# Kernel tuning notes

Measured on AMD Instinct MI355X. Metric: run time of the kernel, lower is better.

The kernel has to match this reference:

```python
import jax, jax.numpy as jnp
import numpy as np

SPATIAL_DIM = 2
N_IN = 4096
N_OUT = 1024
C_IN = 32
C_OUT = 32
FILTER_SEQ = (64, 64)
BATCH = 16


def _grid(num_points):
    # replicates: meshgrid(indexing='xy') of linspace(0,1,n) per dim, dstack, view(-1, d)
    n = int(num_points ** (1.0 / SPATIAL_DIM))
    nodes = np.linspace(0.0, 1.0, n)
    X, Y = np.meshgrid(nodes, nodes, indexing='xy')
    return np.dstack((X, Y)).reshape(-1, SPATIAL_DIM)  # (n^2, 2)


def _cache():
    # replicates QuadConvLayer.cache(): bump-support sparsity pattern
    out_locs = _grid(N_OUT)               # (N_OUT, 2)
    in_nodes = _grid(N_IN)                # (N_IN, 2)
    locs = out_locs[:, None, :] - in_nodes[None, :, :]   # (N_OUT, N_IN, 2)
    bump_arg = np.linalg.norm(locs, axis=2) ** 4
    decay_param = (N_IN / 16.0) ** 2
    mask = bump_arg <= 1.0 / decay_param
    idx = np.argwhere(mask)               # (E, 2), row-major sorted like torch.nonzero
    eval_locs = locs[mask]                # (E, 2)
    return eval_locs.astype(np.float32), idx.astype(np.int64)


def setup_inputs() -> dict:
    key = jax.random.key(0)
    k_feat, k1, k2, k3 = jax.random.split(key, 4)
    eval_locs, eval_indices = _cache()
    # filter MLP G: Linear(2,64,bias=False) -> Sin -> Linear(64,64) -> Sin -> Linear(64, C_IN*C_OUT)
    d0, d1, d2, d3 = SPATIAL_DIM, FILTER_SEQ[0], FILTER_SEQ[1], C_IN * C_OUT
    W1 = jax.random.normal(k1, (d0, d1), jnp.float32) / np.sqrt(d0)
    W2 = jax.random.normal(k2, (d1, d2), jnp.float32) / np.sqrt(d1)
    W3 = jax.random.normal(k3, (d2, d3), jnp.float32) / np.sqrt(d2)
    features = jax.random.normal(k_feat, (BATCH, C_IN, N_IN), jnp.float32)
    return {
        "features": features,
        "W1": W1,
        "W2": W2,
        "W3": W3,
        "eval_locs": jnp.asarray(eval_locs),
        "eval_indices": jnp.asarray(eval_indices),
    }


def reference(features, W1, W2, W3, eval_locs, eval_indices):
    B = features.shape[0]
    E = eval_locs.shape[0]
    seg = eval_indices[:, 0]   # output point per edge (sorted)
    src = eval_indices[:, 1]   # input point per edge
    # filter MLP with Sin activations: (E, 2) -> (E, C_IN, C_OUT)
    h = jnp.sin(eval_locs @ W1)
    h = jnp.sin(h @ W2)
    filt = (h @ W3).reshape(E, C_IN, C_OUT)
    # gather features at source points: (B, C_IN, E)
    gathered = features[:, :, src]
    # faithful to torch: a raw reshape (NOT a transpose) of (B, C_IN, E) -> (B, E, C_IN)
    g = gathered.reshape(B, E, C_IN)
    vals = jnp.einsum('bni,nij->bnj', g, filt)   # (B, E, C_OUT)
    # faithful raw reshape (B, E, C_OUT) -> (B, C_OUT, E)
    vals = vals.reshape(B, C_OUT, E)
    # scatter-sum over edges into output points (segment_coo sum)
    integral = jnp.zeros((B, C_OUT, N_OUT), features.dtype).at[:, :, seg].add(vals)
    return integral
```

## Files before the change

kernel.cpp:

```cpp
#include <hip/hip_runtime.h>
#include <hip/hip_bf16.h>

typedef __bf16 bf16x4  __attribute__((ext_vector_type(4)));
typedef __bf16 bf16x8  __attribute__((ext_vector_type(8)));
typedef __bf16 bf16x16 __attribute__((ext_vector_type(16)));
typedef float  f32x4   __attribute__((ext_vector_type(4)));

#define N_IN   4096
#define N_OUT  1024
#define BATCH  16
#define ROWS   16

#define H1_STR   72
#define H2_STR   72
#define FT_JSTR  40
#define FTH_NSTR 648
#define G_STR    520
#define V_STR    520
#define GSTR2    1048
#define VSTR2    1288
#define FB_FT_NSTR 1288
#define SEG_STR  34

#define WS_W3T_OFF    0
#define WS_W2T_OFF    131072
#define WS_FEATT_OFF  139264
#define WS_NEED       4333568

__global__ void qc_zero_kernel(float* __restrict__ out, int n4) {
    int i = blockIdx.x * blockDim.x + threadIdx.x;
    if (i < n4) ((float4*)out)[i] = make_float4(0.f, 0.f, 0.f, 0.f);
}

__global__ void qc_prep_kernel(const float* __restrict__ w3, const float* __restrict__ w2,
                               __bf16* __restrict__ w3t, __bf16* __restrict__ w2t) {
    int gid = blockIdx.x * blockDim.x + threadIdx.x;
    if (gid < 65536) {
        int k = gid & 63, col = gid >> 6;
        w3t[gid] = (__bf16)w3[k * 1024 + col];
    } else {
        int j = gid - 65536;
        int k = j & 63, col = j >> 6;
        w2t[j] = (__bf16)w2[k * 64 + col];
    }
}

__global__ void qc_prep2_kernel(const float* __restrict__ w3, const float* __restrict__ w2,
                                const float* __restrict__ feat,
                                float* __restrict__ out,
                                __bf16* __restrict__ w3t, __bf16* __restrict__ w2t,
                                __bf16* __restrict__ featT) {
    int bid = blockIdx.x, tid = threadIdx.x;
    if (bid < 512) {
        int i = bid * 256 + tid;
        ((float4*)out)[i] = make_float4(0.f, 0.f, 0.f, 0.f);
    } else if (bid < 768) {
        int gid = (bid - 512) * 256 + tid;
        int k = gid & 63, col = gid >> 6;
        w3t[gid] = (__bf16)w3[k * 1024 + col];
    } else if (bid < 784) {
        int j = (bid - 768) * 256 + tid;
        int k = j & 63, col = j >> 6;
        w2t[j] = (__bf16)w2[k * 64 + col];
    } else {
        int bid2 = bid - 784;
        int c    = bid2 >> 4;
        int src  = (bid2 & 15) * 256 + tid;
        bf16x16 v;
        #pragma unroll
        for (int b = 0; b < 16; ++b)
            v[b] = (__bf16)feat[(b * 32 + c) * N_IN + src];
        __bf16* p = &featT[((size_t)c * N_IN + src) * 16];
        *(bf16x8*)p       = *(bf16x8*)&v;
        *(bf16x8*)(p + 8) = *((bf16x8*)&v + 1);
    }
}

__global__ __launch_bounds__(512, 2)
void qc_fused32_kernel(const __bf16* __restrict__ featT,
                       const float* __restrict__ w1,
                       const float* __restrict__ locs,
                       const int*   __restrict__ eidx,
                       const __bf16* __restrict__ w2t,
                       const __bf16* __restrict__ w3t,
                       float* __restrict__ out,
                       int E)
{
    __shared__ __align__(16) unsigned char region1[41472];
    __shared__ __align__(16) __bf16 h1b[32 * H1_STR];
    __shared__ __align__(16) __bf16 h2b[32 * H2_STR];
    __shared__ unsigned short seg_s[32 * SEG_STR];

    __bf16* gb   = (__bf16*)region1;
    __bf16* ftv  = (__bf16*)region1;
    __bf16* vals = (__bf16*)region1;

    const int tid  = threadIdx.x;
    const int lane = tid & 63;
    const int wv   = tid >> 6;
    const int n0   = blockIdx.x * 32;
    const int t0   = n0 * 32;
    const int ch0  = t0 / E;
    const int m0   = t0 - ch0 * E;

    const int tlb = wv * 128 + lane;
    bf16x16 gvv[2];
    #pragma unroll
    for (int h = 0; h < 2; ++h) {
        int tl = tlb + h * 64;
        int mm = m0 + tl;
        int cc = ch0 + (mm >= E);
        if (mm >= E) mm -= E;
        int2 p = ((const int2*)eidx)[mm];
        seg_s[(tl >> 5) * SEG_STR + (tl & 31)] = (unsigned short)p.x;
        int ccc = cc < 32 ? cc : 31;
        bf16x16 g = *(const bf16x16*)&featT[((size_t)ccc * N_IN + p.y) * 16];
        if (cc >= 32) {
            #pragma unroll
            for (int z = 0; z < 16; ++z) g[z] = (__bf16)0.f;
        }
        gvv[h] = g;
    }

    {
        const int r  = tid >> 4;
        const int j0 = (tid & 15) * 4;
        float lx = 0.f, ly = 0.f;
        int n = n0 + r;
        if (n < E) { lx = locs[n * 2]; ly = locs[n * 2 + 1]; }
        float4 wa = *(const float4*)&w1[j0];
        float4 wb = *(const float4*)&w1[64 + j0];
        __bf16* hp = &h1b[r * H1_STR + j0];
        hp[0] = (__bf16)__sinf(lx * wa.x + ly * wb.x);
        hp[1] = (__bf16)__sinf(lx * wa.y + ly * wb.y);
        hp[2] = (__bf16)__sinf(lx * wa.z + ly * wb.z);
        hp[3] = (__bf16)__sinf(lx * wa.w + ly * wb.w);
    }
    __syncthreads();

    const int ml = lane & 15;
    const int q  = lane >> 4;

    {
        const int rg = (wv >> 2) * 16;
        const int cw = (wv & 3) * 16;
        bf16x8 a0 = *(const bf16x8*)&h1b[(rg + ml) * H1_STR + q * 8];
        bf16x8 a1 = *(const bf16x8*)&h1b[(rg + ml) * H1_STR + 32 + q * 8];
        const __bf16* wp = &w2t[(cw + ml) * 64 + q * 8];
        bf16x8 b0 = *(const bf16x8*)wp;
        bf16x8 b1 = *(const bf16x8*)(wp + 32);
        f32x4 c = {0.f, 0.f, 0.f, 0.f};
        c = __builtin_amdgcn_mfma_f32_16x16x32_bf16(a0, b0, c, 0, 0, 0);
        c = __builtin_amdgcn_mfma_f32_16x16x32_bf16(a1, b1, c, 0, 0, 0);
        #pragma unroll
        for (int g_ = 0; g_ < 4; ++g_)
            h2b[(rg + q * 4 + g_) * H2_STR + cw + ml] = (__bf16)__sinf(c[g_]);
    }

    #pragma unroll
    for (int b = 0; b < 16; ++b) {
        gb[b * GSTR2 + tlb]      = gvv[0][b];
        gb[b * GSTR2 + tlb + 64] = gvv[1][b];
    }
    bf16x8 ag[4];
    #pragma unroll
    for (int rr = 0; rr < 4; ++rr)
        ag[rr] = *(const bf16x8*)&gb[ml * GSTR2 + (wv * 4 + rr) * 32 + q * 8];
    __syncthreads();

    bf16x8 ha00 = *(const bf16x8*)&h2b[ml * H2_STR + q * 8];
    bf16x8 ha01 = *(const bf16x8*)&h2b[ml * H2_STR + 32 + q * 8];
    bf16x8 ha10 = *(const bf16x8*)&h2b[(16 + ml) * H2_STR + q * 8];
    bf16x8 ha11 = *(const bf16x8*)&h2b[(16 + ml) * H2_STR + 32 + q * 8];

    f32x4 c0[4], c1[4];

    {
        f32x4 accA[4], accB[4];
        #pragma unroll
        for (int tt = 0; tt < 4; ++tt) {
            int i_  = wv * 4 + tt;
            int col = i_ * 32 + ml;
            const __bf16* wp = &w3t[col * 64 + q * 8];
            bf16x8 b0 = *(const bf16x8*)wp;
            bf16x8 b1 = *(const bf16x8*)(wp + 32);
            f32x4 cA = {0.f, 0.f, 0.f, 0.f};
            f32x4 cB = {0.f, 0.f, 0.f, 0.f};
            cA = __builtin_amdgcn_mfma_f32_16x16x32_bf16(ha00, b0, cA, 0, 0, 0);
            cA = __builtin_amdgcn_mfma_f32_16x16x32_bf16(ha01, b1, cA, 0, 0, 0);
            cB = __builtin_amdgcn_mfma_f32_16x16x32_bf16(ha10, b0, cB, 0, 0, 0);
            cB = __builtin_amdgcn_mfma_f32_16x16x32_bf16(ha11, b1, cB, 0, 0, 0);
            accA[tt] = cA; accB[tt] = cB;
        }
        #pragma unroll
        for (int g_ = 0; g_ < 4; ++g_) {
            bf16x4 pa, pb;
            #pragma unroll
            for (int tt = 0; tt < 4; ++tt) {
                pa[tt] = (__bf16)accA[tt][g_];
                pb[tt] = (__bf16)accB[tt][g_];
            }
            *(bf16x4*)&ftv[(q * 4 + g_) * FTH_NSTR + ml * FT_JSTR + wv * 4]        = pa;
            *(bf16x4*)&ftv[(16 + q * 4 + g_) * FTH_NSTR + ml * FT_JSTR + wv * 4]   = pb;
        }
    }
    __syncthreads();

    {
        bf16x8 f[4];
        #pragma unroll
        for (int rr = 0; rr < 4; ++rr)
            f[rr] = *(const bf16x8*)&ftv[(wv * 4 + rr) * FTH_NSTR + ml * FT_JSTR + q * 8];
        #pragma unroll
        for (int rr = 0; rr < 4; ++rr) {
            f32x4 z = {0.f, 0.f, 0.f, 0.f};
            c0[rr] = __builtin_amdgcn_mfma_f32_16x16x32_bf16(ag[rr], f[rr], z, 0, 0, 0);
        }
    }
    __syncthreads();

    {
        f32x4 accA[4], accB[4];
        #pragma unroll
        for (int tt = 0; tt < 4; ++tt) {
            int i_  = wv * 4 + tt;
            int col = i_ * 32 + 16 + ml;
            const __bf16* wp = &w3t[col * 64 + q * 8];
            bf16x8 b0 = *(const bf16x8*)wp;
            bf16x8 b1 = *(const bf16x8*)(wp + 32);
            f32x4 cA = {0.f, 0.f, 0.f, 0.f};
            f32x4 cB = {0.f, 0.f, 0.f, 0.f};
            cA = __builtin_amdgcn_mfma_f32_16x16x32_bf16(ha00, b0, cA, 0, 0, 0);
            cA = __builtin_amdgcn_mfma_f32_16x16x32_bf16(ha01, b1, cA, 0, 0, 0);
            cB = __builtin_amdgcn_mfma_f32_16x16x32_bf16(ha10, b0, cB, 0, 0, 0);
            cB = __builtin_amdgcn_mfma_f32_16x16x32_bf16(ha11, b1, cB, 0, 0, 0);
            accA[tt] = cA; accB[tt] = cB;
        }
        #pragma unroll
        for (int g_ = 0; g_ < 4; ++g_) {
            bf16x4 pa, pb;
            #pragma unroll
            for (int tt = 0; tt < 4; ++tt) {
                pa[tt] = (__bf16)accA[tt][g_];
                pb[tt] = (__bf16)accB[tt][g_];
            }
            *(bf16x4*)&ftv[(q * 4 + g_) * FTH_NSTR + ml * FT_JSTR + wv * 4]        = pa;
            *(bf16x4*)&ftv[(16 + q * 4 + g_) * FTH_NSTR + ml * FT_JSTR + wv * 4]   = pb;
        }
    }
    __syncthreads();

    bf16x8 f1[4];
    #pragma unroll
    for (int rr = 0; rr < 4; ++rr)
        f1[rr] = *(const bf16x8*)&ftv[(wv * 4 + rr) * FTH_NSTR + ml * FT_JSTR + q * 8];
    __syncthreads();
    #pragma unroll
    for (int rr = 0; rr < 4; ++rr) {
        f32x4 z = {0.f, 0.f, 0.f, 0.f};
        c1[rr] = __builtin_amdgcn_mfma_f32_16x16x32_bf16(ag[rr], f1[rr], z, 0, 0, 0);
    }
    #pragma unroll
    for (int rr = 0; rr < 4; ++rr) {
        int r = wv * 4 + rr;
        __bf16* vp = &vals[r * FT_JSTR];
        #pragma unroll
        for (int g_ = 0; g_ < 4; ++g_) {
            int b = q * 4 + g_;
            vp[b * VSTR2 + ml]      = (__bf16)c0[rr][g_];
            vp[b * VSTR2 + 16 + ml] = (__bf16)c1[rr][g_];
        }
    }
    __syncthreads();

    {
        const int b   = tid >> 5;
        const int w   = tid & 31;
        const int tl0 = w * 32;
        const __bf16* vp = &vals[b * VSTR2 + w * FT_JSTR];
        bf16x8 v0 = *(const bf16x8*)(vp);
        bf16x8 v1 = *(const bf16x8*)(vp + 8);
        bf16x8 v2 = *(const bf16x8*)(vp + 16);
        bf16x8 v3 = *(const bf16x8*)(vp + 24);
        float vv[32];
        #pragma unroll
        for (int j = 0; j < 8; ++j) {
            vv[j]      = (float)v0[j];
            vv[8 + j]  = (float)v1[j];
            vv[16 + j] = (float)v2[j];
            vv[24 + j] = (float)v3[j];
        }
        int key_prev = -1;
        float acc = 0.f;
        #pragma unroll
        for (int j = 0; j < 32; ++j) {
            int mm2 = m0 + tl0 + j;
            int cc2 = ch0 + (mm2 >= E);
            if (cc2 < 32) {
                int o   = (int)seg_s[w * SEG_STR + j];
                int key = (cc2 << 10) | o;
                if (key != key_prev) {
                    if (key_prev >= 0) atomicAdd(&out[(b << 15) + key_prev], acc);
                    key_prev = key;
                    acc = vv[j];
                } else {
                    acc += vv[j];
                }
            }
        }
        if (key_prev >= 0) atomicAdd(&out[(b << 15) + key_prev], acc);
    }
}

__global__ __launch_bounds__(256, 2)
void qc_main_kernel(const float* __restrict__ feat,
                    const float* __restrict__ w1,
                    const float* __restrict__ w2,
                    const float* __restrict__ locs,
                    const int*   __restrict__ eidx,
                    const __bf16* __restrict__ w3t,
                    float* __restrict__ out,
                    int E)
{
    __shared__ __align__(16) __bf16 h1b[ROWS * H1_STR];
    __shared__ __align__(16) __bf16 h2b[ROWS * H2_STR];
    __shared__ __align__(16) __bf16 ftv[ROWS * FB_FT_NSTR];
    __shared__ __align__(16) __bf16 gb [BATCH * G_STR];
    __shared__ unsigned short seg_s[512];
    __shared__ unsigned short src_s[512];

    const int tid = threadIdx.x;
    const int n0  = blockIdx.x * ROWS;
    const int t0  = n0 * 32;
    const int ch0 = t0 / E;
    const int m0  = t0 - ch0 * E;

    {
        const int r  = tid >> 4;
        const int j0 = (tid & 15) * 4;
        float lx = 0.f, ly = 0.f;
        int n = n0 + r;
        if (n < E) { lx = locs[n * 2]; ly = locs[n * 2 + 1]; }
        float4 wa = *(const float4*)&w1[j0];
        float4 wb = *(const float4*)&w1[64 + j0];
        __bf16* h = &h1b[r * H1_STR + j0];
        h[0] = (__bf16)__sinf(lx * wa.x + ly * wb.x);
        h[1] = (__bf16)__sinf(lx * wa.y + ly * wb.y);
        h[2] = (__bf16)__sinf(lx * wa.z + ly * wb.z);
        h[3] = (__bf16)__sinf(lx * wa.w + ly * wb.w);
    }
    for (int tl = tid; tl < 512; tl += 256) {
        int mm = m0 + tl; if (mm >= E) mm -= E;
        seg_s[tl] = (unsigned short)eidx[mm * 2];
        src_s[tl] = (unsigned short)eidx[mm * 2 + 1];
    }
    __syncthreads();

    {
        const int r  = tid >> 4;
        const int j0 = (tid & 15) * 4;
        float a0 = 0.f, a1 = 0.f, a2 = 0.f, a3 = 0.f;
        const __bf16* h1r = &h1b[r * H1_STR];
        #pragma unroll 8
        for (int k = 0; k < 64; ++k) {
            float h = (float)h1r[k];
            float4 w = *(const float4*)&w2[k * 64 + j0];
            a0 += h * w.x; a1 += h * w.y; a2 += h * w.z; a3 += h * w.w;
        }
        __bf16* h = &h2b[r * H2_STR + j0];
        h[0] = (__bf16)__sinf(a0);
        h[1] = (__bf16)__sinf(a1);
        h[2] = (__bf16)__sinf(a2);
        h[3] = (__bf16)__sinf(a3);
    }
    #pragma unroll 4
    for (int it = 0; it < 32; ++it) {
        int idx = it * 256 + tid;
        int b   = idx >> 9;
        int tl  = idx & 511;
        int mm  = m0 + tl;
        int cc  = ch0 + (mm >= E);
        if (mm >= E) mm -= E;
        float v = 0.f;
        if (cc < 32) v = feat[(b * 32 + cc) * N_IN + (int)src_s[tl]];
        gb[b * G_STR + tl] = (__bf16)v;
    }
    __syncthreads();

    const int lane = tid & 63;
    const int wv   = tid >> 6;
    const int ml   = lane & 15;
    const int q    = lane >> 4;

    {
        bf16x8 a0 = *(const bf16x8*)&h2b[ml * H2_STR + q * 8];
        bf16x8 a1 = *(const bf16x8*)&h2b[ml * H2_STR + 32 + q * 8];
        #pragma unroll
        for (int t = 0; t < 16; ++t) {
            int col = wv * 256 + t * 16 + ml;
            const __bf16* wp = &w3t[col * 64 + q * 8];
            bf16x8 b0 = *(const bf16x8*)wp;
            bf16x8 b1 = *(const bf16x8*)(wp + 32);
            f32x4 c = {0.f, 0.f, 0.f, 0.f};
            c = __builtin_amdgcn_mfma_f32_16x16x32_bf16(a0, b0, c, 0, 0, 0);
            c = __builtin_amdgcn_mfma_f32_16x16x32_bf16(a1, b1, c, 0, 0, 0);
            int i_ = col >> 5, j_ = col & 31;
            __bf16* fp = &ftv[j_ * FT_JSTR + i_];
            fp[(q * 4 + 0) * FB_FT_NSTR] = (__bf16)c[0];
            fp[(q * 4 + 1) * FB_FT_NSTR] = (__bf16)c[1];
            fp[(q * 4 + 2) * FB_FT_NSTR] = (__bf16)c[2];
            fp[(q * 4 + 3) * FB_FT_NSTR] = (__bf16)c[3];
        }
    }
    __syncthreads();

    {
        bf16x8 ag[4], f0[4], f1[4];
        #pragma unroll
        for (int rr = 0; rr < 4; ++rr) {
            int r = wv * 4 + rr;
            ag[rr] = *(const bf16x8*)&gb[ml * G_STR + r * 32 + q * 8];
            f0[rr] = *(const bf16x8*)&ftv[r * FB_FT_NSTR + ml        * FT_JSTR + q * 8];
            f1[rr] = *(const bf16x8*)&ftv[r * FB_FT_NSTR + (16 + ml) * FT_JSTR + q * 8];
        }
        __syncthreads();
        __bf16* valsb = ftv;
        #pragma unroll
        for (int rr = 0; rr < 4; ++rr) {
            int r = wv * 4 + rr;
            f32x4 c0 = {0.f, 0.f, 0.f, 0.f};
            f32x4 c1 = {0.f, 0.f, 0.f, 0.f};
            c0 = __builtin_amdgcn_mfma_f32_16x16x32_bf16(ag[rr], f0[rr], c0, 0, 0, 0);
            c1 = __builtin_amdgcn_mfma_f32_16x16x32_bf16(ag[rr], f1[rr], c1, 0, 0, 0);
            __bf16* vp = &valsb[r * 32];
            #pragma unroll
            for (int g_ = 0; g_ < 4; ++g_) {
                int b = q * 4 + g_;
                vp[b * V_STR + ml]      = (__bf16)c0[g_];
                vp[b * V_STR + 16 + ml] = (__bf16)c1[g_];
            }
        }
    }
    __syncthreads();

    {
        const __bf16* valsb = ftv;
        const int b = tid >> 4;
        const int r = tid & 15;
        const __bf16* vp = &valsb[b * V_STR + r * 32];
        bf16x8 v0 = *(const bf16x8*)(vp);
        bf16x8 v1 = *(const bf16x8*)(vp + 8);
        bf16x8 v2 = *(const bf16x8*)(vp + 16);
        bf16x8 v3 = *(const bf16x8*)(vp + 24);
        float vv[32];
        #pragma unroll
        for (int j = 0; j < 8; ++j) {
            vv[j]      = (float)v0[j];
            vv[8 + j]  = (float)v1[j];
            vv[16 + j] = (float)v2[j];
            vv[24 + j] = (float)v3[j];
        }
        const int tl0 = r * 32;
        int key_prev = -1;
        float acc = 0.f;
        #pragma unroll
        for (int j = 0; j < 32; ++j) {
            int mm = m0 + tl0 + j;
            int cc = ch0 + (mm >= E);
            if (mm >= E) mm -= E;
            if (cc < 32) {
                int o   = (int)seg_s[tl0 + j];
                int key = ((b * 32 + cc) << 10) | o;
                if (key != key_prev) {
                    if (key_prev >= 0) atomicAdd(&out[key_prev], acc);
                    key_prev = key;
                    acc = vv[j];
                } else {
                    acc += vv[j];
                }
            }
        }
        if (key_prev >= 0) atomicAdd(&out[key_prev], acc);
    }
}

extern "C" void kernel_launch(void* const* d_in, const int* in_sizes, int n_in,
                              void* d_out, int out_size, void* d_ws, size_t ws_size,
                              hipStream_t stream)
{
    (void)n_in;
    const float* feat = (const float*)d_in[0];
    const float* w1   = (const float*)d_in[1];
    const float* w2   = (const float*)d_in[2];
    const float* w3   = (const float*)d_in[3];
    const float* locs = (const float*)d_in[4];
    const int*   eidx = (const int*)d_in[5];
    float* out  = (float*)d_out;

    const int E = in_sizes[4] / 2;
    if (E <= 0) return;

    __bf16* w3t   = (__bf16*)((char*)d_ws + WS_W3T_OFF);
    __bf16* w2t   = (__bf16*)((char*)d_ws + WS_W2T_OFF);
    __bf16* featT = (__bf16*)((char*)d_ws + WS_FEATT_OFF);

    if (ws_size >= (size_t)WS_NEED) {
        int nblocks = (E + 31) / 32;
        qc_prep2_kernel<<<1296, 256, 0, stream>>>(w3, w2, feat, out, w3t, w2t, featT);
        qc_fused32_kernel<<<nblocks, 512, 0, stream>>>(featT, w1, locs, eidx, w2t, w3t, out, E);
    } else {
        int n4 = out_size / 4;
        int nblocks = (E + ROWS - 1) / ROWS;
        qc_zero_kernel<<<(n4 + 255) / 256, 256, 0, stream>>>(out, n4);
        qc_prep_kernel<<<272, 256, 0, stream>>>(w3, w2, w3t, w2t);
        qc_main_kernel<<<nblocks, 256, 0, stream>>>(feat, w1, w2, locs, eidx, w3t, out, E);
    }
}
```

Measured before the change: 134.0 us.

## Process two tiles per block with prefetch of next tile's gathers

Each block of the fused kernel now loops over two 32-edge tiles instead of one. W1 and W2 fragments are hoisted out of the loop, and the gather and location loads for the next tile are issued before the scatter-atomic phase of the current tile so their latency overlaps. The launch bound is raised to 4 blocks per CU, and the per-edge channel/key computation in the scatter loop is simplified to a precomputed crossing point. Risks include higher register pressure from the 4-wave occupancy bound, possible spills, and half as many blocks in the grid.

```diff
diff --git a/kernel.cpp b/kernel.cpp
--- a/kernel.cpp
+++ b/kernel.cpp
@@ -21,6 +21,7 @@
 #define VSTR2    1288
 #define FB_FT_NSTR 1288
 #define SEG_STR  34
+#define TPB      2
 
 #define WS_W3T_OFF    0
 #define WS_W2T_OFF    131072
@@ -76,7 +77,7 @@
     }
 }
 
-__global__ __launch_bounds__(512, 2)
+__global__ __launch_bounds__(512, 4)
 void qc_fused32_kernel(const __bf16* __restrict__ featT,
                        const float* __restrict__ w1,
                        const float* __restrict__ locs,
@@ -84,7 +85,7 @@
                        const __bf16* __restrict__ w2t,
                        const __bf16* __restrict__ w3t,
                        float* __restrict__ out,
-                       int E)
+                       int E, int nt)
 {
     __shared__ __align__(16) unsigned char region1[41472];
     __shared__ __align__(16) __bf16 h1b[32 * H1_STR];
@@ -98,217 +99,240 @@
     const int tid  = threadIdx.x;
     const int lane = tid & 63;
     const int wv   = tid >> 6;
-    const int n0   = blockIdx.x * 32;
-    const int t0   = n0 * 32;
-    const int ch0  = t0 / E;
-    const int m0   = t0 - ch0 * E;
-
-    const int tlb = wv * 128 + lane;
-    bf16x16 gvv[2];
-    #pragma unroll
-    for (int h = 0; h < 2; ++h) {
-        int tl = tlb + h * 64;
-        int mm = m0 + tl;
-        int cc = ch0 + (mm >= E);
-        if (mm >= E) mm -= E;
-        int2 p = ((const int2*)eidx)[mm];
-        seg_s[(tl >> 5) * SEG_STR + (tl & 31)] = (unsigned short)p.x;
-        int ccc = cc < 32 ? cc : 31;
-        bf16x16 g = *(const bf16x16*)&featT[((size_t)ccc * N_IN + p.y) * 16];
-        if (cc >= 32) {
-            #pragma unroll
-            for (int z = 0; z < 16; ++z) g[z] = (__bf16)0.f;
-        }
-        gvv[h] = g;
-    }
-
-    {
-        const int r  = tid >> 4;
-        const int j0 = (tid & 15) * 4;
-        float lx = 0.f, ly = 0.f;
-        int n = n0 + r;
+    const int ml   = lane & 15;
+    const int q    = lane >> 4;
+    const int tlb  = wv * 128 + lane;
+
+    const int rA = tid >> 4;
+    const int jA = (tid & 15) * 4;
+    const float4 wa = *(const float4*)&w1[jA];
+    const float4 wb = *(const float4*)&w1[64 + jA];
+    const int rg = (wv >> 2) * 16;
+    const int cw = (wv & 3) * 16;
+    const bf16x8 bw0 = *(const bf16x8*)&w2t[(cw + ml) * 64 + q * 8];
+    const bf16x8 bw1 = *(const bf16x8*)&w2t[(cw + ml) * 64 + 32 + q * 8];
+
+    int tb = blockIdx.x * TPB;
+
+    bf16x16 gvv[2]; int sg0 = 0, sg1 = 0; float lx = 0.f, ly = 0.f;
+
+    auto prefetch = [&](int tbn) {
+        const int t0p  = tbn << 10;
+        const int ch0p = t0p / E;
+        const int m0p  = t0p - ch0p * E;
+        #pragma unroll
+        for (int h = 0; h < 2; ++h) {
+            int tl = tlb + h * 64;
+            int mm = m0p + tl;
+            int cc = ch0p + (mm >= E);
+            if (mm >= E) mm -= E;
+            int2 p = ((const int2*)eidx)[mm];
+            int ccc = cc < 32 ? cc : 31;
+            bf16x16 g = *(const bf16x16*)&featT[((size_t)ccc * N_IN + p.y) * 16];
+            if (cc >= 32) {
+                #pragma unroll
+                for (int z = 0; z < 16; ++z) g[z] = (__bf16)0.f;
+            }
+            gvv[h] = g;
+            if (h == 0) sg0 = p.x; else sg1 = p.x;
+        }
+        int n = (tbn << 5) + rA;
+        lx = 0.f; ly = 0.f;
         if (n < E) { lx = locs[n * 2]; ly = locs[n * 2 + 1]; }
-        float4 wa = *(const float4*)&w1[j0];
-        float4 wb = *(const float4*)&w1[64 + j0];
-        __bf16* hp = &h1b[r * H1_STR + j0];
-        hp[0] = (__bf16)__sinf(lx * wa.x + ly * wb.x);
-        hp[1] = (__bf16)__sinf(lx * wa.y + ly * wb.y);
-        hp[2] = (__bf16)__sinf(lx * wa.z + ly * wb.z);
-        hp[3] = (__bf16)__sinf(lx * wa.w + ly * wb.w);
-    }
-    __syncthreads();
-
-    const int ml = lane & 15;
-    const int q  = lane >> 4;
-
-    {
-        const int rg = (wv >> 2) * 16;
-        const int cw = (wv & 3) * 16;
-        bf16x8 a0 = *(const bf16x8*)&h1b[(rg + ml) * H1_STR + q * 8];
-        bf16x8 a1 = *(const bf16x8*)&h1b[(rg + ml) * H1_STR + 32 + q * 8];
-        const __bf16* wp = &w2t[(cw + ml) * 64 + q * 8];
-        bf16x8 b0 = *(const bf16x8*)wp;
-        bf16x8 b1 = *(const bf16x8*)(wp + 32);
-        f32x4 c = {0.f, 0.f, 0.f, 0.f};
-        c = __builtin_amdgcn_mfma_f32_16x16x32_bf16(a0, b0, c, 0, 0, 0);
-        c = __builtin_amdgcn_mfma_f32_16x16x32_bf16(a1, b1, c, 0, 0, 0);
-        #pragma unroll
-        for (int g_ = 0; g_ < 4; ++g_)
-            h2b[(rg + q * 4 + g_) * H2_STR + cw + ml] = (__bf16)__sinf(c[g_]);
-    }
-
-    #pragma unroll
-    for (int b = 0; b < 16; ++b) {
-        gb[b * GSTR2 + tlb]      = gvv[0][b];
-        gb[b * GSTR2 + tlb + 64] = gvv[1][b];
-    }
-    bf16x8 ag[4];
-    #pragma unroll
-    for (int rr = 0; rr < 4; ++rr)
-        ag[rr] = *(const bf16x8*)&gb[ml * GSTR2 + (wv * 4 + rr) * 32 + q * 8];
-    __syncthreads();
-
-    bf16x8 ha00 = *(const bf16x8*)&h2b[ml * H2_STR + q * 8];
-    bf16x8 ha01 = *(const bf16x8*)&h2b[ml * H2_STR + 32 + q * 8];
-    bf16x8 ha10 = *(const bf16x8*)&h2b[(16 + ml) * H2_STR + q * 8];
-    bf16x8 ha11 = *(const bf16x8*)&h2b[(16 + ml) * H2_STR + 32 + q * 8];
-
-    f32x4 c0[4], c1[4];
-
-    {
-        f32x4 accA[4], accB[4];
-        #pragma unroll
-        for (int tt = 0; tt < 4; ++tt) {
-            int i_  = wv * 4 + tt;
-            int col = i_ * 32 + ml;
-            const __bf16* wp = &w3t[col * 64 + q * 8];
-            bf16x8 b0 = *(const bf16x8*)wp;
-            bf16x8 b1 = *(const bf16x8*)(wp + 32);
-            f32x4 cA = {0.f, 0.f, 0.f, 0.f};
-            f32x4 cB = {0.f, 0.f, 0.f, 0.f};
-            cA = __builtin_amdgcn_mfma_f32_16x16x32_bf16(ha00, b0, cA, 0, 0, 0);
-            cA = __builtin_amdgcn_mfma_f32_16x16x32_bf16(ha01, b1, cA, 0, 0, 0);
-            cB = __builtin_amdgcn_mfma_f32_16x16x32_bf16(ha10, b0, cB, 0, 0, 0);
-            cB = __builtin_amdgcn_mfma_f32_16x16x32_bf16(ha11, b1, cB, 0, 0, 0);
-            accA[tt] = cA; accB[tt] = cB;
-        }
-        #pragma unroll
-        for (int g_ = 0; g_ < 4; ++g_) {
-            bf16x4 pa, pb;
+    };
+
+    prefetch(tb);
+
+    for (int it = 0; it < TPB; ++it, ++tb) {
+        if (tb >= nt) break;
+        const int t0  = tb << 10;
+        const int ch0 = t0 / E;
+        const int m0  = t0 - ch0 * E;
+
+        {
+            __bf16* hp = &h1b[rA * H1_STR + jA];
+            hp[0] = (__bf16)__sinf(lx * wa.x + ly * wb.x);
+            hp[1] = (__bf16)__sinf(lx * wa.y + ly * wb.y);
+            hp[2] = (__bf16)__sinf(lx * wa.z + ly * wb.z);
+            hp[3] = (__bf16)__sinf(lx * wa.w + ly * wb.w);
+        }
+        __syncthreads();
+
+        {
+            bf16x8 a0 = *(const bf16x8*)&h1b[(rg + ml) * H1_STR + q * 8];
+            bf16x8 a1 = *(const bf16x8*)&h1b[(rg + ml) * H1_STR + 32 + q * 8];
+            f32x4 c = {0.f, 0.f, 0.f, 0.f};
+            c = __builtin_amdgcn_mfma_f32_16x16x32_bf16(a0, bw0, c, 0, 0, 0);
+            c = __builtin_amdgcn_mfma_f32_16x16x32_bf16(a1, bw1, c, 0, 0, 0);
+            #pragma unroll
+            for (int g_ = 0; g_ < 4; ++g_)
+                h2b[(rg + q * 4 + g_) * H2_STR + cw + ml] = (__bf16)__sinf(c[g_]);
+        }
+
+        #pragma unroll
+        for (int b = 0; b < 16; ++b) {
+            gb[b * GSTR2 + tlb]      = gvv[0][b];
+            gb[b * GSTR2 + tlb + 64] = gvv[1][b];
+        }
+        seg_s[(tlb >> 5) * SEG_STR + (tlb & 31)] = (unsigned short)sg0;
+        {
+            int tl1 = tlb + 64;
+            seg_s[(tl1 >> 5) * SEG_STR + (tl1 & 31)] = (unsigned short)sg1;
+        }
+        bf16x8 ag[4];
+        #pragma unroll
+        for (int rr = 0; rr < 4; ++rr)
+            ag[rr] = *(const bf16x8*)&gb[ml * GSTR2 + (wv * 4 + rr) * 32 + q * 8];
+        __syncthreads();
+
+        bf16x8 ha00 = *(const bf16x8*)&h2b[ml * H2_STR + q * 8];
+        bf16x8 ha01 = *(const bf16x8*)&h2b[ml * H2_STR + 32 + q * 8];
+        bf16x8 ha10 = *(const bf16x8*)&h2b[(16 + ml) * H2_STR + q * 8];
+        bf16x8 ha11 = *(const bf16x8*)&h2b[(16 + ml) * H2_STR + 32 + q * 8];
+
+        f32x4 c0[4], c1[4];
+
+        {
+            f32x4 accA[4], accB[4];
             #pragma unroll
             for (int tt = 0; tt < 4; ++tt) {
-                pa[tt] = (__bf16)accA[tt][g_];
-                pb[tt] = (__bf16)accB[tt][g_];
-            }
-            *(bf16x4*)&ftv[(q * 4 + g_) * FTH_NSTR + ml * FT_JSTR + wv * 4]        = pa;
-            *(bf16x4*)&ftv[(16 + q * 4 + g_) * FTH_NSTR + ml * FT_JSTR + wv * 4]   = pb;
-        }
-    }
-    __syncthreads();
-
-    {
-        bf16x8 f[4];
+                int i_  = wv * 4 + tt;
+                int col = i_ * 32 + ml;
+                const __bf16* wp = &w3t[col * 64 + q * 8];
+                bf16x8 b0 = *(const bf16x8*)wp;
+                bf16x8 b1 = *(const bf16x8*)(wp + 32);
+                f32x4 cA = {0.f, 0.f, 0.f, 0.f};
+                f32x4 cB = {0.f, 0.f, 0.f, 0.f};
+                cA = __builtin_amdgcn_mfma_f32_16x16x32_bf16(ha00, b0, cA, 0, 0, 0);
+                cA = __builtin_amdgcn_mfma_f32_16x16x32_bf16(ha01, b1, cA, 0, 0, 0);
+                cB = __builtin_amdgcn_mfma_f32_16x16x32_bf16(ha10, b0, cB, 0, 0, 0);
+                cB = __builtin_amdgcn_mfma_f32_16x16x32_bf16(ha11, b1, cB, 0, 0, 0);
+                accA[tt] = cA; accB[tt] = cB;
+            }
+            #pragma unroll
+            for (int g_ = 0; g_ < 4; ++g_) {
+                bf16x4 pa, pb;
+                #pragma unroll
+                for (int tt = 0; tt < 4; ++tt) {
+                    pa[tt] = (__bf16)accA[tt][g_];
+                    pb[tt] = (__bf16)accB[tt][g_];
+                }
+                *(bf16x4*)&ftv[(q * 4 + g_) * FTH_NSTR + ml * FT_JSTR + wv * 4]        = pa;
+                *(bf16x4*)&ftv[(16 + q * 4 + g_) * FTH_NSTR + ml * FT_JSTR + wv * 4]   = pb;
+            }
+        }
+        __syncthreads();
+
+        {
+            bf16x8 f[4];
+            #pragma unroll
+            for (int rr = 0; rr < 4; ++rr)
+                f[rr] = *(const bf16x8*)&ftv[(wv * 4 + rr) * FTH_NSTR + ml * FT_JSTR + q * 8];
+            #pragma unroll
+            for (int rr = 0; rr < 4; ++rr) {
+                f32x4 z = {0.f, 0.f, 0.f, 0.f};
+                c0[rr] = __builtin_amdgcn_mfma_f32_16x16x32_bf16(ag[rr], f[rr], z, 0, 0, 0);
+            }
+        }
+        __syncthreads();
+
+        {
+            f32x4 accA[4], accB[4];
+            #pragma unroll
+            for (int tt = 0; tt < 4; ++tt) {
+                int i_  = wv * 4 + tt;
+                int col = i_ * 32 + 16 + ml;
+                const __bf16* wp = &w3t[col * 64 + q * 8];
+                bf16x8 b0 = *(const bf16x8*)wp;
+                bf16x8 b1 = *(const bf16x8*)(wp + 32);
+                f32x4 cA = {0.f, 0.f, 0.f, 0.f};
+                f32x4 cB = {0.f, 0.f, 0.f, 0.f};
+                cA = __builtin_amdgcn_mfma_f32_16x16x32_bf16(ha00, b0, cA, 0, 0, 0);
+                cA = __builtin_amdgcn_mfma_f32_16x16x32_bf16(ha01, b1, cA, 0, 0, 0);
+                cB = __builtin_amdgcn_mfma_f32_16x16x32_bf16(ha10, b0, cB, 0, 0, 0);
+                cB = __builtin_amdgcn_mfma_f32_16x16x32_bf16(ha11, b1, cB, 0, 0, 0);
+                accA[tt] = cA; accB[tt] = cB;
+            }
+            #pragma unroll
+            for (int g_ = 0; g_ < 4; ++g_) {
+                bf16x4 pa, pb;
+                #pragma unroll
+                for (int tt = 0; tt < 4; ++tt) {
+                    pa[tt] = (__bf16)accA[tt][g_];
+                    pb[tt] = (__bf16)accB[tt][g_];
+                }
+                *(bf16x4*)&ftv[(q * 4 + g_) * FTH_NSTR + ml * FT_JSTR + wv * 4]        = pa;
+                *(bf16x4*)&ftv[(16 + q * 4 + g_) * FTH_NSTR + ml * FT_JSTR + wv * 4]   = pb;
+            }
+        }
+        __syncthreads();
+
+        bf16x8 f1[4];
         #pragma unroll
         for (int rr = 0; rr < 4; ++rr)
-            f[rr] = *(const bf16x8*)&ftv[(wv * 4 + rr) * FTH_NSTR + ml * FT_JSTR + q * 8];
+            f1[rr] = *(const bf16x8*)&ftv[(wv * 4 + rr) * FTH_NSTR + ml * FT_JSTR + q * 8];
+        __syncthreads();
         #pragma unroll
         for (int rr = 0; rr < 4; ++rr) {
             f32x4 z = {0.f, 0.f, 0.f, 0.f};
-            c0[rr] = __builtin_amdgcn_mfma_f32_16x16x32_bf16(ag[rr], f[rr], z, 0, 0, 0);
-        }
-    }
-    __syncthreads();
-
-    {
-        f32x4 accA[4], accB[4];
-        #pragma unroll
-        for (int tt = 0; tt < 4; ++tt) {
-            int i_  = wv * 4 + tt;
-            int col = i_ * 32 + 16 + ml;
-            const __bf16* wp = &w3t[col * 64 + q * 8];
-            bf16x8 b0 = *(const bf16x8*)wp;
-            bf16x8 b1 = *(const bf16x8*)(wp + 32);
-            f32x4 cA = {0.f, 0.f, 0.f, 0.f};
-            f32x4 cB = {0.f, 0.f, 0.f, 0.f};
-            cA = __builtin_amdgcn_mfma_f32_16x16x32_bf16(ha00, b0, cA, 0, 0, 0);
-            cA = __builtin_amdgcn_mfma_f32_16x16x32_bf16(ha01, b1, cA, 0, 0, 0);
-            cB = __builtin_amdgcn_mfma_f32_16x16x32_bf16(ha10, b0, cB, 0, 0, 0);
-            cB = __builtin_amdgcn_mfma_f32_16x16x32_bf16(ha11, b1, cB, 0, 0, 0);
-            accA[tt] = cA; accB[tt] = cB;
-        }
-        #pragma unroll
-        for (int g_ = 0; g_ < 4; ++g_) {
-            bf16x4 pa, pb;
-            #pragma unroll
-            for (int tt = 0; tt < 4; ++tt) {
-                pa[tt] = (__bf16)accA[tt][g_];
-                pb[tt] = (__bf16)accB[tt][g_];
-            }
-            *(bf16x4*)&ftv[(q * 4 + g_) * FTH_NSTR + ml * FT_JSTR + wv * 4]        = pa;
-            *(bf16x4*)&ftv[(16 + q * 4 + g_) * FTH_NSTR + ml * FT_JSTR + wv * 4]   = pb;
-        }
-    }
-    __syncthreads();
-
-    bf16x8 f1[4];
-    #pragma unroll
-    for (int rr = 0; rr < 4; ++rr)
-        f1[rr] = *(const bf16x8*)&ftv[(wv * 4 + rr) * FTH_NSTR + ml * FT_JSTR + q * 8];
-    __syncthreads();
-    #pragma unroll
-    for (int rr = 0; rr < 4; ++rr) {
-        f32x4 z = {0.f, 0.f, 0.f, 0.f};
-        c1[rr] = __builtin_amdgcn_mfma_f32_16x16x32_bf16(ag[rr], f1[rr], z, 0, 0, 0);
-    }
-    #pragma unroll
-    for (int rr = 0; rr < 4; ++rr) {
-        int r = wv * 4 + rr;
-        __bf16* vp = &vals[r * FT_JSTR];
-        #pragma unroll
-        for (int g_ = 0; g_ < 4; ++g_) {
-            int b = q * 4 + g_;
-            vp[b * VSTR2 + ml]      = (__bf16)c0[rr][g_];
-            vp[b * VSTR2 + 16 + ml] = (__bf16)c1[rr][g_];
-        }
-    }
-    __syncthreads();
-
-    {
-        const int b   = tid >> 5;
-        const int w   = tid & 31;
-        const int tl0 = w * 32;
-        const __bf16* vp = &vals[b * VSTR2 + w * FT_JSTR];
-        bf16x8 v0 = *(const bf16x8*)(vp);
-        bf16x8 v1 = *(const bf16x8*)(vp + 8);
-        bf16x8 v2 = *(const bf16x8*)(vp + 16);
-        bf16x8 v3 = *(const bf16x8*)(vp + 24);
-        float vv[32];
-        #pragma unroll
-        for (int j = 0; j < 8; ++j) {
-            vv[j]      = (float)v0[j];
-            vv[8 + j]  = (float)v1[j];
-            vv[16 + j] = (float)v2[j];
-            vv[24 + j] = (float)v3[j];
-        }
-        int key_prev = -1;
-        float acc = 0.f;
-        #pragma unroll
-        for (int j = 0; j < 32; ++j) {
-            int mm2 = m0 + tl0 + j;
-            int cc2 = ch0 + (mm2 >= E);
-            if (cc2 < 32) {
-                int o   = (int)seg_s[w * SEG_STR + j];
-                int key = (cc2 << 10) | o;
-                if (key != key_prev) {
-                    if (key_prev >= 0) atomicAdd(&out[(b << 15) + key_prev], acc);
-                    key_prev = key;
-                    acc = vv[j];
-                } else {
-                    acc += vv[j];
+            c1[rr] = __builtin_amdgcn_mfma_f32_16x16x32_bf16(ag[rr], f1[rr], z, 0, 0, 0);
+        }
+        #pragma unroll
+        for (int rr = 0; rr < 4; ++rr) {
+            int r = wv * 4 + rr;
+            __bf16* vp = &vals[r * FT_JSTR];
+            #pragma unroll
+            for (int g_ = 0; g_ < 4; ++g_) {
+                int b = q * 4 + g_;
+                vp[b * VSTR2 + ml]      = (__bf16)c0[rr][g_];
+                vp[b * VSTR2 + 16 + ml] = (__bf16)c1[rr][g_];
+            }
+        }
+        __syncthreads();
+
+        {
+            const int be = tid >> 5;
+            const int w  = tid & 31;
+            const __bf16* vp = &vals[be * VSTR2 + w * FT_JSTR];
+            bf16x8 v0 = *(const bf16x8*)(vp);
+            bf16x8 v1 = *(const bf16x8*)(vp + 8);
+            bf16x8 v2 = *(const bf16x8*)(vp + 16);
+            bf16x8 v3 = *(const bf16x8*)(vp + 24);
+
+            if (it + 1 < TPB && tb + 1 < nt) prefetch(tb + 1);
+
+            float vv[32];
+            #pragma unroll
+            for (int j = 0; j < 8; ++j) {
+                vv[j]      = (float)v0[j];
+                vv[8 + j]  = (float)v1[j];
+                vv[16 + j] = (float)v2[j];
+                vv[24 + j] = (float)v3[j];
+            }
+            int mwin = m0 + (w << 5);
+            int cb   = ch0;
+            if (mwin >= E) { mwin -= E; ++cb; }
+            int jcross = E - mwin;
+            int base0 = (cb < 32)     ? ((be << 15) | (cb << 10))       : -1;
+            int base1 = (cb + 1 < 32) ? ((be << 15) | ((cb + 1) << 10)) : -1;
+            int key_prev = -1;
+            float acc = 0.f;
+            #pragma unroll
+            for (int j = 0; j < 32; ++j) {
+                int basej = (j < jcross) ? base0 : base1;
+                if (basej >= 0) {
+                    int key = basej + (int)seg_s[w * SEG_STR + j];
+                    if (key != key_prev) {
+                        if (key_prev >= 0) atomicAdd(&out[key_prev], acc);
+                        key_prev = key;
+                        acc = vv[j];
+                    } else {
+                        acc += vv[j];
+                    }
                 }
             }
-        }
-        if (key_prev >= 0) atomicAdd(&out[(b << 15) + key_prev], acc);
+            if (key_prev >= 0) atomicAdd(&out[key_prev], acc);
+        }
     }
 }
 
@@ -505,9 +529,10 @@
     __bf16* featT = (__bf16*)((char*)d_ws + WS_FEATT_OFF);
 
     if (ws_size >= (size_t)WS_NEED) {
-        int nblocks = (E + 31) / 32;
+        int nt = (E + 31) / 32;
+        int nblocks = (nt + TPB - 1) / TPB;
         qc_prep2_kernel<<<1296, 256, 0, stream>>>(w3, w2, feat, out, w3t, w2t, featT);
-        qc_fused32_kernel<<<nblocks, 512, 0, stream>>>(featT, w1, locs, eidx, w2t, w3t, out, E);
+        qc_fused32_kernel<<<nblocks, 512, 0, stream>>>(featT, w1, locs, eidx, w2t, w3t, out, E, nt);
     } else {
         int n4 = out_size / 4;
         int nblocks = (E + ROWS - 1) / ROWS;
```

Result: slower. 202.0 us (+50.8%).
